# Kernel optimization log

Measured on AMD Instinct MI355X. Metric: run time of the kernel, lower is better.

Reference implementation:

```python
import jax, jax.numpy as jnp
import numpy as np

VOCAB, ENC, DEC, ATT, EMB = 10000, 2048, 512, 512, 512
B, P, L = 64, 196, 20


def setup_inputs() -> dict:
    key = jax.random.key(0)
    ks = jax.random.split(key, 24)
    s = lambda k, shape, fan: jax.random.normal(k, shape, jnp.float32) / np.sqrt(fan)
    inp = {
        "img_features": jax.random.normal(ks[0], (B, P, ENC), jnp.float32),
        "captions": jax.random.randint(ks[1], (B, L), 0, VOCAB),
        # init-state projections
        "W_init_h": s(ks[2], (DEC, ENC), ENC), "b_init_h": jnp.zeros((DEC,), jnp.float32),
        "W_init_c": s(ks[3], (DEC, ENC), ENC), "b_init_c": jnp.zeros((DEC,), jnp.float32),
        # attention
        "W_dec": s(ks[4], (ATT, DEC), DEC), "b_dec": jnp.zeros((ATT,), jnp.float32),
        "W_enc": s(ks[5], (ATT, ENC), ENC), "b_enc": jnp.zeros((ATT,), jnp.float32),
        "W_fin": s(ks[6], (1, ATT), ATT), "b_fin": jnp.zeros((1,), jnp.float32),
        # gate + output + embedding
        "W_gate": s(ks[7], (ENC, DEC), DEC), "b_gate": jnp.zeros((ENC,), jnp.float32),
        "W_out": s(ks[8], (VOCAB, DEC), DEC), "b_out": jnp.zeros((VOCAB,), jnp.float32),
        "emb": s(ks[9], (VOCAB, EMB), EMB),
        # LSTMCell (PyTorch gate order: i, f, g, o)
        "W_ih": s(ks[10], (4 * DEC, EMB + ENC), EMB + ENC), "b_ih": jnp.zeros((4 * DEC,), jnp.float32),
        "W_hh": s(ks[11], (4 * DEC, DEC), DEC), "b_hh": jnp.zeros((4 * DEC,), jnp.float32),
    }
    return inp


def _decode(img_features, captions, W_init_h, b_init_h, W_init_c, b_init_c,
            W_dec, b_dec, W_enc, b_enc, W_fin, b_fin,
            W_gate, b_gate, W_out, b_out, emb, W_ih, W_hh, b_ih, b_hh):
    # lengths are uniform (padded tensor), so sort/restore are identity and
    # batch_size_t == B at every step.
    avg = img_features.mean(axis=1)                              # [B,ENC]
    h0 = jnp.tanh(avg @ W_init_h.T + b_init_h)                   # [B,DEC]
    c0 = jnp.tanh(avg @ W_init_c.T + b_init_c)
    enc_proj = img_features @ W_enc.T + b_enc                    # [B,P,ATT] (loop-invariant)
    emb_seq = emb[captions[:, :-1]]                              # [B,T,EMB], T = L-1

    def step(carry, e_t):
        h, c = carry
        U_h = h @ W_dec.T + b_dec                                # [B,ATT]
        att = jnp.tanh(enc_proj + U_h[:, None, :])               # [B,P,ATT]
        e = (att @ W_fin.T + b_fin)[..., 0]                      # [B,P]
        alpha = jax.nn.softmax(e, axis=1)
        context = jnp.einsum('bpe,bp->be', img_features, alpha)  # [B,ENC]
        gate = jax.nn.sigmoid(h @ W_gate.T + b_gate)             # [B,ENC]
        x = jnp.concatenate([e_t, gate * context], axis=1)       # [B,EMB+ENC]
        gates = x @ W_ih.T + b_ih + h @ W_hh.T + b_hh            # [B,4*DEC]
        i, f, g, o = jnp.split(gates, 4, axis=1)
        c_new = jax.nn.sigmoid(f) * c + jax.nn.sigmoid(i) * jnp.tanh(g)
        h_new = jax.nn.sigmoid(o) * jnp.tanh(c_new)
        out = h_new @ W_out.T + b_out                            # [B,VOCAB] (dropout=eval identity)
        return (h_new, c_new), (out, alpha)

    _, (preds, alphas) = jax.lax.scan(step, (h0, c0), jnp.swapaxes(emb_seq, 0, 1))
    return jnp.swapaxes(preds, 0, 1), jnp.swapaxes(alphas, 0, 1)  # [B,T,VOCAB], [B,T,P]


def reference(img_features, captions, W_init_h, b_init_h, W_init_c, b_init_c,
              W_dec, b_dec, W_enc, b_enc, W_fin, b_fin,
              W_gate, b_gate, W_out, b_out, emb, W_ih, W_hh, b_ih, b_hh):
    return _decode(img_features, captions, W_init_h, b_init_h, W_init_c, b_init_c,
                   W_dec, b_dec, W_enc, b_enc, W_fin, b_fin,
                   W_gate, b_gate, W_out, b_out, emb, W_ih, W_hh, b_ih, b_hh)
```

## Files before the change

### kernel.cpp

```cpp
#include <hip/hip_runtime.h>
#include <hip/hip_bf16.h>

typedef unsigned short u16;
typedef unsigned int   u32;

#define BB    64
#define PP    196
#define ENC   2048
#define DEC   512
#define ATT   512
#define EMB   512
#define VOCAB 10000
#define VPAD2 10112
#define TT    19
#define LCAP  20
#define XDIM  3072
#define LDSTR 40
#define LD64  72

typedef __bf16 bf16x8 __attribute__((ext_vector_type(8)));
typedef float  f32x4  __attribute__((ext_vector_type(4)));

__device__ __forceinline__ float bf2f(u16 u) {
  union { float f; u32 i; } v; v.i = ((u32)u) << 16; return v.f;
}
__device__ __forceinline__ u16 f2bf(float f) {
  u32 x = __float_as_uint(f);
  u32 r = (x + 0x7FFFu + ((x >> 16) & 1u)) >> 16;
  return (u16)r;
}
__device__ __forceinline__ u32 pack2(float a, float b) {
  return (u32)f2bf(a) | ((u32)f2bf(b) << 16);
}
__device__ __forceinline__ float wred_sum(float v) {
  #pragma unroll
  for (int off = 32; off > 0; off >>= 1) v += __shfl_xor(v, off, 64);
  return v;
}
__device__ __forceinline__ float wred_max(float v) {
  #pragma unroll
  for (int off = 32; off > 0; off >>= 1) v = fmaxf(v, __shfl_xor(v, off, 64));
  return v;
}
__device__ __forceinline__ float tanh_fast(float x) {
  return 1.f - 2.f / (__expf(2.f * x) + 1.f);
}
__device__ __forceinline__ float sigm(float x) {
  return 1.f / (1.f + __expf(-x));
}

__global__ __launch_bounds__(256) void k_cvt_simple(u16* __restrict__ dst,
    const float* __restrict__ src, int n4) {
  int stride = gridDim.x * blockDim.x;
  for (int i = blockIdx.x * blockDim.x + threadIdx.x; i < n4; i += stride) {
    float4 v = ((const float4*)src)[i];
    ((uint2*)dst)[i] = make_uint2(pack2(v.x, v.y), pack2(v.z, v.w));
  }
}

__global__ __launch_bounds__(256) void k_cvt_pad(u16* __restrict__ dst,
    const float* __restrict__ src) {
  int total = VPAD2 * (DEC / 2);
  int stride = gridDim.x * blockDim.x;
  for (int i = blockIdx.x * blockDim.x + threadIdx.x; i < total; i += stride) {
    int row = i >> 8, c2 = i & 255;
    u32 v = 0;
    if (row < VOCAB) {
      float2 f = ((const float2*)src)[(size_t)row * 256 + c2];
      v = pack2(f.x, f.y);
    }
    ((u32*)dst)[i] = v;
  }
}

__global__ __launch_bounds__(256) void k_cvt_comb(u16* __restrict__ dst,
    const float* __restrict__ Wih, const float* __restrict__ Whh) {
  int j = blockIdx.x;
  for (int t = threadIdx.x; t < 768; t += 256) {
    int col = t * 4;
    float4 v = (col < 2560)
        ? ((const float4*)(Wih + (size_t)j * 2560))[t]
        : ((const float4*)(Whh + (size_t)j * 512))[(col - 2560) >> 2];
    ((uint2*)(dst + (size_t)j * XDIM))[t] = make_uint2(pack2(v.x, v.y), pack2(v.z, v.w));
  }
}

__global__ __launch_bounds__(256) void k_cvt_dect(u16* __restrict__ dst,
    const float* __restrict__ Wdec) {
  int idx = blockIdx.x * 256 + threadIdx.x;
  int k0 = idx >> 9, j = idx & 511;
  const float* src = Wdec + (size_t)j * DEC + k0 * 8;
  float4 f0 = ((const float4*)src)[0];
  float4 f1 = ((const float4*)src)[1];
  ((uint4*)dst)[idx] = make_uint4(pack2(f0.x, f0.y), pack2(f0.z, f0.w),
                                  pack2(f1.x, f1.y), pack2(f1.z, f1.w));
}

__global__ __launch_bounds__(256) void k_avg(const float* __restrict__ img,
    u16* __restrict__ avgb) {
  int b = blockIdx.x;
  int col = blockIdx.y * 256 + threadIdx.x;
  const float* base = img + (size_t)b * PP * ENC + col;
  float s = 0.f;
  for (int p = 0; p < PP; ++p) s += base[(size_t)p * ENC];
  avgb[b * ENC + col] = f2bf(s * (1.f / PP));
}

__global__ __launch_bounds__(256) void k_init_mfma(const u16* __restrict__ avgb,
    const u16* __restrict__ Winitb, const float* __restrict__ bh,
    const float* __restrict__ bc, u16* __restrict__ h, float* __restrict__ c) {
  __shared__ __align__(16) u16 As[2 * 64 * LD64];
  __shared__ __align__(16) u16 Bs[2 * 64 * LD64];
  int n0 = blockIdx.x * 64;
  int tid = threadIdx.x, wv = tid >> 6, lane = tid & 63;
  int wm = wv >> 1, wn = wv & 1;
  int fr = lane & 15, kg = (lane >> 4) * 8, rq = lane >> 4;
  int r0 = tid >> 3, kc0 = (tid & 7) * 8;
  int r1 = (tid + 256) >> 3, kc1 = ((tid + 256) & 7) * 8;
  uint4 pa0 = *(const uint4*)&avgb[(size_t)r0 * ENC + kc0];
  uint4 pa1 = *(const uint4*)&avgb[(size_t)r1 * ENC + kc1];
  uint4 pb0 = *(const uint4*)&Winitb[(size_t)(n0 + r0) * ENC + kc0];
  uint4 pb1 = *(const uint4*)&Winitb[(size_t)(n0 + r1) * ENC + kc1];
  f32x4 acc[2][2] = {};
  const int NK = ENC / 64;
  for (int kt = 0; kt < NK; ++kt) {
    u16* as = As + (kt & 1) * (64 * LD64);
    u16* bs = Bs + (kt & 1) * (64 * LD64);
    *(uint4*)&as[r0 * LD64 + kc0] = pa0;
    *(uint4*)&as[r1 * LD64 + kc1] = pa1;
    *(uint4*)&bs[r0 * LD64 + kc0] = pb0;
    *(uint4*)&bs[r1 * LD64 + kc1] = pb1;
    __syncthreads();
    if (kt + 1 < NK) {
      int k0 = (kt + 1) * 64;
      pa0 = *(const uint4*)&avgb[(size_t)r0 * ENC + k0 + kc0];
      pa1 = *(const uint4*)&avgb[(size_t)r1 * ENC + k0 + kc1];
      pb0 = *(const uint4*)&Winitb[(size_t)(n0 + r0) * ENC + k0 + kc0];
      pb1 = *(const uint4*)&Winitb[(size_t)(n0 + r1) * ENC + k0 + kc1];
    }
    #pragma unroll
    for (int ks = 0; ks < 2; ++ks) {
      bf16x8 a0 = *(const bf16x8*)&as[(wm * 32 + fr) * LD64 + ks * 32 + kg];
      bf16x8 a1 = *(const bf16x8*)&as[(wm * 32 + 16 + fr) * LD64 + ks * 32 + kg];
      bf16x8 b0 = *(const bf16x8*)&bs[(wn * 32 + fr) * LD64 + ks * 32 + kg];
      bf16x8 b1 = *(const bf16x8*)&bs[(wn * 32 + 16 + fr) * LD64 + ks * 32 + kg];
      acc[0][0] = __builtin_amdgcn_mfma_f32_16x16x32_bf16(a0, b0, acc[0][0], 0, 0, 0);
      acc[0][1] = __builtin_amdgcn_mfma_f32_16x16x32_bf16(a0, b1, acc[0][1], 0, 0, 0);
      acc[1][0] = __builtin_amdgcn_mfma_f32_16x16x32_bf16(a1, b0, acc[1][0], 0, 0, 0);
      acc[1][1] = __builtin_amdgcn_mfma_f32_16x16x32_bf16(a1, b1, acc[1][1], 0, 0, 0);
    }
  }
  #pragma unroll
  for (int mi = 0; mi < 2; ++mi)
    for (int ni = 0; ni < 2; ++ni)
      #pragma unroll
      for (int r = 0; r < 4; ++r) {
        int m = wm * 32 + mi * 16 + rq * 4 + r;
        int n = n0 + wn * 32 + ni * 16 + fr;
        float v = acc[mi][ni][r];
        if (n < DEC) h[m * DEC + n] = f2bf(tanh_fast(v + bh[n]));
        else         c[m * DEC + (n - DEC)] = tanh_fast(v + bc[n - DEC]);
      }
}

template <int SRC>
__global__ __launch_bounds__(256) void k_encproj(
    const u16* __restrict__ Ab, const float* __restrict__ Af,
    const u16* __restrict__ Wb, const float* __restrict__ Wf,
    const float* __restrict__ benc, u16* __restrict__ epj) {
  __shared__ __align__(16) u16 As[128 * LDSTR];
  __shared__ __align__(16) u16 Bs[128 * LDSTR];
  int m0 = blockIdx.x * 128, n0 = blockIdx.y * 128;
  int tid = threadIdx.x, wv = tid >> 6, lane = tid & 63;
  int wm = wv >> 1, wn = wv & 1;
  int fr = lane & 15, kg = (lane >> 4) * 8, rq = lane >> 4;
  f32x4 acc[4][4] = {};
  for (int k0 = 0; k0 < ENC; k0 += 32) {
    __syncthreads();
    #pragma unroll
    for (int i = 0; i < 2; ++i) {
      int id = tid + i * 256;
      int r = id >> 2, kc = id & 3;
      if (SRC == 0) {
        *(uint4*)(&As[r * LDSTR + kc * 8]) = *(const uint4*)(&Ab[(size_t)(m0 + r) * ENC + k0 + kc * 8]);
        *(uint4*)(&Bs[r * LDSTR + kc * 8]) = *(const uint4*)(&Wb[(size_t)(n0 + r) * ENC + k0 + kc * 8]);
      } else {
        const float* asrc = &Af[(size_t)(m0 + r) * ENC + k0 + kc * 8];
        float4 f0 = ((const float4*)asrc)[0];
        float4 f1 = ((const float4*)asrc)[1];
        *(uint4*)(&As[r * LDSTR + kc * 8]) =
            make_uint4(pack2(f0.x, f0.y), pack2(f0.z, f0.w),
                       pack2(f1.x, f1.y), pack2(f1.z, f1.w));
        const float* bsrc = &Wf[(size_t)(n0 + r) * ENC + k0 + kc * 8];
        float4 g0 = ((const float4*)bsrc)[0];
        float4 g1 = ((const float4*)bsrc)[1];
        *(uint4*)(&Bs[r * LDSTR + kc * 8]) =
            make_uint4(pack2(g0.x, g0.y), pack2(g0.z, g0.w),
                       pack2(g1.x, g1.y), pack2(g1.z, g1.w));
      }
    }
    __syncthreads();
    bf16x8 af[4], bfr[4];
    #pragma unroll
    for (int i = 0; i < 4; ++i) {
      af[i]  = *(const bf16x8*)(&As[(wm * 64 + i * 16 + fr) * LDSTR + kg]);
      bfr[i] = *(const bf16x8*)(&Bs[(wn * 64 + i * 16 + fr) * LDSTR + kg]);
    }
    #pragma unroll
    for (int mi = 0; mi < 4; ++mi)
      #pragma unroll
      for (int ni = 0; ni < 4; ++ni)
        acc[mi][ni] = __builtin_amdgcn_mfma_f32_16x16x32_bf16(af[mi], bfr[ni], acc[mi][ni], 0, 0, 0);
  }
  #pragma unroll
  for (int mi = 0; mi < 4; ++mi)
    for (int ni = 0; ni < 4; ++ni)
      #pragma unroll
      for (int r = 0; r < 4; ++r) {
        int m = m0 + wm * 64 + mi * 16 + rq * 4 + r;
        int n = n0 + wn * 64 + ni * 16 + fr;
        epj[(size_t)m * ATT + n] = f2bf(acc[mi][ni][r] + benc[n]);
      }
}

__global__ __launch_bounds__(256) void k_logits(const u16* __restrict__ hall,
    const u16* __restrict__ Woutb2, const float* __restrict__ bout,
    float* __restrict__ preds) {
  __shared__ __align__(16) u16 As[128 * LDSTR];
  __shared__ __align__(16) u16 Bs[128 * LDSTR];
  int m0 = blockIdx.x * 128, n0 = blockIdx.y * 128;
  int tid = threadIdx.x, wv = tid >> 6, lane = tid & 63;
  int wm = wv >> 1, wn = wv & 1;
  int fr = lane & 15, kg = (lane >> 4) * 8, rq = lane >> 4;
  f32x4 acc[4][4] = {};
  for (int k0 = 0; k0 < DEC; k0 += 32) {
    __syncthreads();
    #pragma unroll
    for (int i = 0; i < 2; ++i) {
      int id = tid + i * 256;
      int r = id >> 2, kc = id & 3;
      *(uint4*)(&As[r * LDSTR + kc * 8]) = *(const uint4*)(&hall[(size_t)(m0 + r) * DEC + k0 + kc * 8]);
      *(uint4*)(&Bs[r * LDSTR + kc * 8]) = *(const uint4*)(&Woutb2[(size_t)(n0 + r) * DEC + k0 + kc * 8]);
    }
    __syncthreads();
    bf16x8 af[4], bfr[4];
    #pragma unroll
    for (int i = 0; i < 4; ++i) {
      af[i]  = *(const bf16x8*)(&As[(wm * 64 + i * 16 + fr) * LDSTR + kg]);
      bfr[i] = *(const bf16x8*)(&Bs[(wn * 64 + i * 16 + fr) * LDSTR + kg]);
    }
    #pragma unroll
    for (int mi = 0; mi < 4; ++mi)
      #pragma unroll
      for (int ni = 0; ni < 4; ++ni)
        acc[mi][ni] = __builtin_amdgcn_mfma_f32_16x16x32_bf16(af[mi], bfr[ni], acc[mi][ni], 0, 0, 0);
  }
  #pragma unroll
  for (int mi = 0; mi < 4; ++mi)
    for (int ni = 0; ni < 4; ++ni)
      #pragma unroll
      for (int r = 0; r < 4; ++r) {
        int m = m0 + wm * 64 + mi * 16 + rq * 4 + r;
        int n = n0 + wn * 64 + ni * 16 + fr;
        if (m < TT * BB && n < VOCAB) {
          int t = m >> 6, b = m & 63;
          preds[(size_t)b * (TT * VOCAB) + (size_t)t * VOCAB + n] = acc[mi][ni][r] + bout[n];
        }
      }
}

__global__ __launch_bounds__(512) void k_front(const u16* __restrict__ h,
    const u16* __restrict__ WdecT2, const float* __restrict__ bdec,
    const u16* __restrict__ Wgateb, const float* __restrict__ bgate,
    const u16* __restrict__ epj, const float* __restrict__ wfin,
    const float* __restrict__ bfin, const int* __restrict__ captions,
    const float* __restrict__ emb,
    float* __restrict__ gate, float* __restrict__ e_ws,
    u16* __restrict__ x, float* __restrict__ alphas, int step) {
  __shared__ __align__(16) u16 smem[2 * 64 * LD64 + 2 * 128 * LD64];
  int bid = blockIdx.x;
  int tid = threadIdx.x, wv = tid >> 6, lane = tid & 63;

  if (bid >= 64) {
    u16* As = smem;
    u16* Bs = smem + 2 * 64 * LD64;
    int n0 = (bid - 64) * 128;
    int wm = wv >> 2, wn = wv & 3;
    int fr = lane & 15, kgr = (lane >> 4) * 8, rq = lane >> 4;
    int r0 = tid >> 3, kc0 = (tid & 7) * 8;
    uint4 pa  = *(const uint4*)&h[(size_t)r0 * DEC + kc0];
    uint4 pb0 = *(const uint4*)&Wgateb[(size_t)(n0 + r0) * DEC + kc0];
    uint4 pb1 = *(const uint4*)&Wgateb[(size_t)(n0 + 64 + r0) * DEC + kc0];
    f32x4 acc[2][2] = {};
    const int NK = DEC / 64;
    for (int kt = 0; kt < NK; ++kt) {
      u16* as = As + (kt & 1) * (64 * LD64);
      u16* bs = Bs + (kt & 1) * (128 * LD64);
      *(uint4*)&as[r0 * LD64 + kc0] = pa;
      *(uint4*)&bs[r0 * LD64 + kc0] = pb0;
      *(uint4*)&bs[(64 + r0) * LD64 + kc0] = pb1;
      __syncthreads();
      if (kt + 1 < NK) {
        int k0 = (kt + 1) * 64;
        pa  = *(const uint4*)&h[(size_t)r0 * DEC + k0 + kc0];
        pb0 = *(const uint4*)&Wgateb[(size_t)(n0 + r0) * DEC + k0 + kc0];
        pb1 = *(const uint4*)&Wgateb[(size_t)(n0 + 64 + r0) * DEC + k0 + kc0];
      }
      #pragma unroll
      for (int ks = 0; ks < 2; ++ks) {
        bf16x8 a0 = *(const bf16x8*)&as[(wm * 32 + fr) * LD64 + ks * 32 + kgr];
        bf16x8 a1 = *(const bf16x8*)&as[(wm * 32 + 16 + fr) * LD64 + ks * 32 + kgr];
        bf16x8 b0 = *(const bf16x8*)&bs[(wn * 32 + fr) * LD64 + ks * 32 + kgr];
        bf16x8 b1 = *(const bf16x8*)&bs[(wn * 32 + 16 + fr) * LD64 + ks * 32 + kgr];
        acc[0][0] = __builtin_amdgcn_mfma_f32_16x16x32_bf16(a0, b0, acc[0][0], 0, 0, 0);
        acc[0][1] = __builtin_amdgcn_mfma_f32_16x16x32_bf16(a0, b1, acc[0][1], 0, 0, 0);
        acc[1][0] = __builtin_amdgcn_mfma_f32_16x16x32_bf16(a1, b0, acc[1][0], 0, 0, 0);
        acc[1][1] = __builtin_amdgcn_mfma_f32_16x16x32_bf16(a1, b1, acc[1][1], 0, 0, 0);
      }
    }
    #pragma unroll
    for (int mi = 0; mi < 2; ++mi)
      for (int ni = 0; ni < 2; ++ni)
        #pragma unroll
        for (int r = 0; r < 4; ++r) {
          int m = wm * 32 + mi * 16 + rq * 4 + r;
          int n = n0 + wn * 32 + ni * 16 + fr;
          gate[m * ENC + n] = sigm(acc[mi][ni][r] + bgate[n]);
        }
    return;
  }

  float* s_h  = (float*)smem;
  float* s_uh = s_h + DEC;
  float* s_wf = s_uh + ATT;
  float* s_e  = s_wf + ATT;
  int b = bid;
  s_h[tid] = bf2f(h[b * DEC + tid]);
  s_wf[tid] = wfin[tid];
  if (tid < 256) {
    int capv = captions[b * LCAP + step];
    float2 f = ((const float2*)(emb + (size_t)capv * EMB))[tid];
    ((u32*)(x + (size_t)b * XDIM))[tid] = pack2(f.x, f.y);
    ((u32*)(x + (size_t)b * XDIM + 2560))[tid] = ((const u32*)(h + (size_t)b * DEC))[tid];
  }
  __syncthreads();
  {
    float acc = bdec[tid];
    #pragma unroll 4
    for (int k0 = 0; k0 < 64; ++k0) {
      bf16x8 wrow = *(const bf16x8*)&WdecT2[(size_t)(k0 * 512 + tid) * 8];
      #pragma unroll
      for (int kk = 0; kk < 8; ++kk)
        acc += s_h[k0 * 8 + kk] * (float)wrow[kk];
    }
    s_uh[tid] = acc;
  }
  __syncthreads();
  float b0 = bfin[0];
  for (int p = wv; p < PP; p += 8) {
    const u16* row = epj + (size_t)(b * PP + p) * ATT;
    float acc = 0.f;
    #pragma unroll
    for (int ki = 0; ki < 8; ++ki) {
      int a = lane + ki * 64;
      acc += tanh_fast(bf2f(row[a]) + s_uh[a]) * s_wf[a];
    }
    acc = wred_sum(acc);
    if (lane == 0) s_e[p] = acc + b0;
  }
  __syncthreads();
  if (tid < 64) {
    float v0 = s_e[tid], v1 = s_e[tid + 64], v2 = s_e[tid + 128];
    float v3 = (tid + 192 < PP) ? s_e[tid + 192] : -1e30f;
    float m = wred_max(fmaxf(fmaxf(v0, v1), fmaxf(v2, v3)));
    float e0 = __expf(v0 - m), e1 = __expf(v1 - m), e2 = __expf(v2 - m);
    float e3 = (tid + 192 < PP) ? __expf(v3 - m) : 0.f;
    float inv = 1.f / wred_sum(e0 + e1 + e2 + e3);
    s_e[tid] = e0 * inv; s_e[tid + 64] = e1 * inv; s_e[tid + 128] = e2 * inv;
    if (tid + 192 < PP) s_e[tid + 192] = e3 * inv;
  }
  __syncthreads();
  if (tid < PP) {
    float a = s_e[tid];
    alphas[(size_t)b * (TT * PP) + (size_t)step * PP + tid] = a;
    e_ws[b * PP + tid] = a;
  }
}

template <int SRC>
__global__ __launch_bounds__(256) void k_ctx(const float* __restrict__ e_ws,
    const float* __restrict__ gate, const u16* __restrict__ imgb,
    const float* __restrict__ imgf, u16* __restrict__ x) {
  __shared__ float s_a[PP];
  int b = blockIdx.x, et = blockIdx.y;
  int tid = threadIdx.x;
  if (tid < PP) s_a[tid] = e_ws[b * PP + tid];
  __syncthreads();
  int e0i = et * 512 + tid * 2;
  float c0 = 0.f, c1 = 0.f;
  if (SRC == 0) {
    const u16* ib = imgb + (size_t)b * PP * ENC + e0i;
    for (int p = 0; p < PP; ++p) {
      u32 v = *(const u32*)(ib + (size_t)p * ENC);
      float ap = s_a[p];
      c0 += ap * bf2f((u16)(v & 0xFFFF));
      c1 += ap * bf2f((u16)(v >> 16));
    }
  } else {
    const float* ib = imgf + (size_t)b * PP * ENC + e0i;
    for (int p = 0; p < PP; ++p) {
      float2 v = *(const float2*)(ib + (size_t)p * ENC);
      float ap = s_a[p];
      c0 += ap * v.x;
      c1 += ap * v.y;
    }
  }
  float g0 = gate[b * ENC + e0i], g1 = gate[b * ENC + e0i + 1];
  *(u32*)(&x[(size_t)b * XDIM + 512 + e0i]) = pack2(c0 * g0, c1 * g1);
}

__global__ __launch_bounds__(256) void k_lstm_part(const u16* __restrict__ x,
    const u16* __restrict__ Wcomb, float* __restrict__ pbuf) {
  __shared__ __align__(16) u16 As[2 * 64 * LD64];
  __shared__ __align__(16) u16 Bs[2 * 64 * LD64];
  int jt = blockIdx.x, ksp = blockIdx.y;
  int kbase = ksp * 768;
  int tid = threadIdx.x, wv = tid >> 6, lane = tid & 63;
  int wm = wv >> 1, wn = wv & 1;
  int fr = lane & 15, kg = (lane >> 4) * 8, rq = lane >> 4;
  int r0 = tid >> 3, kc0 = (tid & 7) * 8;
  int r1 = (tid + 256) >> 3, kc1 = ((tid + 256) & 7) * 8;
  int wrow0 = (r0 >> 4) * 512 + jt * 16 + (r0 & 15);
  int wrow1 = (r1 >> 4) * 512 + jt * 16 + (r1 & 15);
  uint4 pa0 = *(const uint4*)&x[(size_t)r0 * XDIM + kbase + kc0];
  uint4 pa1 = *(const uint4*)&x[(size_t)r1 * XDIM + kbase + kc1];
  uint4 pb0 = *(const uint4*)&Wcomb[(size_t)wrow0 * XDIM + kbase + kc0];
  uint4 pb1 = *(const uint4*)&Wcomb[(size_t)wrow1 * XDIM + kbase + kc1];
  f32x4 acc[2][2] = {};
  const int NK = 12;
  for (int kt = 0; kt < NK; ++kt) {
    u16* as = As + (kt & 1) * (64 * LD64);
    u16* bs = Bs + (kt & 1) * (64 * LD64);
    *(uint4*)&as[r0 * LD64 + kc0] = pa0;
    *(uint4*)&as[r1 * LD64 + kc1] = pa1;
    *(uint4*)&bs[r0 * LD64 + kc0] = pb0;
    *(uint4*)&bs[r1 * LD64 + kc1] = pb1;
    __syncthreads();
    if (kt + 1 < NK) {
      int k0 = kbase + (kt + 1) * 64;
      pa0 = *(const uint4*)&x[(size_t)r0 * XDIM + k0 + kc0];
      pa1 = *(const uint4*)&x[(size_t)r1 * XDIM + k0 + kc1];
      pb0 = *(const uint4*)&Wcomb[(size_t)wrow0 * XDIM + k0 + kc0];
      pb1 = *(const uint4*)&Wcomb[(size_t)wrow1 * XDIM + k0 + kc1];
    }
    #pragma unroll
    for (int ks = 0; ks < 2; ++ks) {
      bf16x8 a0 = *(const bf16x8*)&as[(wm * 32 + fr) * LD64 + ks * 32 + kg];
      bf16x8 a1 = *(const bf16x8*)&as[(wm * 32 + 16 + fr) * LD64 + ks * 32 + kg];
      bf16x8 b0 = *(const bf16x8*)&bs[(wn * 32 + fr) * LD64 + ks * 32 + kg];
      bf16x8 b1 = *(const bf16x8*)&bs[(wn * 32 + 16 + fr) * LD64 + ks * 32 + kg];
      acc[0][0] = __builtin_amdgcn_mfma_f32_16x16x32_bf16(a0, b0, acc[0][0], 0, 0, 0);
      acc[0][1] = __builtin_amdgcn_mfma_f32_16x16x32_bf16(a0, b1, acc[0][1], 0, 0, 0);
      acc[1][0] = __builtin_amdgcn_mfma_f32_16x16x32_bf16(a1, b0, acc[1][0], 0, 0, 0);
      acc[1][1] = __builtin_amdgcn_mfma_f32_16x16x32_bf16(a1, b1, acc[1][1], 0, 0, 0);
    }
  }
  float* pout = pbuf + (size_t)(ksp * 32 + jt) * 4096;
  #pragma unroll
  for (int mi = 0; mi < 2; ++mi)
    for (int ni = 0; ni < 2; ++ni)
      #pragma unroll
      for (int r = 0; r < 4; ++r) {
        int m = wm * 32 + mi * 16 + rq * 4 + r;
        int n = wn * 32 + ni * 16 + fr;
        pout[m * 64 + n] = acc[mi][ni][r];
      }
}

__global__ __launch_bounds__(256) void k_lstm_fin(const float* __restrict__ pbuf,
    const float* __restrict__ bih, const float* __restrict__ bhh,
    float* __restrict__ c, u16* __restrict__ h, u16* __restrict__ hall, int step) {
  int jt = blockIdx.x, tid = threadIdx.x;
  #pragma unroll
  for (int ii = 0; ii < 4; ++ii) {
    int idx = tid + ii * 256;
    int bb = idx >> 4, jj = idx & 15;
    int j = jt * 16 + jj;
    float g4[4];
    #pragma unroll
    for (int g = 0; g < 4; ++g) {
      float s = 0.f;
      #pragma unroll
      for (int ks = 0; ks < 4; ++ks)
        s += pbuf[(size_t)(ks * 32 + jt) * 4096 + bb * 64 + g * 16 + jj];
      g4[g] = s;
    }
    float iv = g4[0] + bih[j]        + bhh[j];
    float fv = g4[1] + bih[512 + j]  + bhh[512 + j];
    float gv = g4[2] + bih[1024 + j] + bhh[1024 + j];
    float ov = g4[3] + bih[1536 + j] + bhh[1536 + j];
    float co = c[bb * DEC + j];
    float cn = sigm(fv) * co + sigm(iv) * tanh_fast(gv);
    float hn = sigm(ov) * tanh_fast(cn);
    c[bb * DEC + j] = cn;
    u16 hb = f2bf(hn);
    h[bb * DEC + j] = hb;
    hall[(size_t)(step * BB + bb) * DEC + j] = hb;
  }
}

extern "C" void kernel_launch(void* const* d_in, const int* in_sizes, int n_in,
                              void* d_out, int out_size, void* d_ws, size_t ws_size,
                              hipStream_t stream) {
  const float* img   = (const float*)d_in[0];
  const int*   cap   = (const int*)  d_in[1];
  const float* Winh  = (const float*)d_in[2];
  const float* binh  = (const float*)d_in[3];
  const float* Winc  = (const float*)d_in[4];
  const float* binc  = (const float*)d_in[5];
  const float* Wdec  = (const float*)d_in[6];
  const float* bdec  = (const float*)d_in[7];
  const float* Wenc  = (const float*)d_in[8];
  const float* benc  = (const float*)d_in[9];
  const float* Wfin  = (const float*)d_in[10];
  const float* bfin  = (const float*)d_in[11];
  const float* Wgate = (const float*)d_in[12];
  const float* bgate = (const float*)d_in[13];
  const float* Wout  = (const float*)d_in[14];
  const float* bout  = (const float*)d_in[15];
  const float* emb   = (const float*)d_in[16];
  const float* Wih   = (const float*)d_in[17];
  const float* bih   = (const float*)d_in[18];
  const float* Whh   = (const float*)d_in[19];
  const float* bhh   = (const float*)d_in[20];

  char* ws = (char*)d_ws;
  u16*   epj    = (u16*)  (ws);
  u16*   Winitb = (u16*)  (ws);
  u16*   avgb   = (u16*)  (ws + 4194304);
  u16*   Wcomb  = (u16*)  (ws + 12845056);
  u16*   Woutb2 = (u16*)  (ws + 25427968);
  u16*   Wgateb = (u16*)  (ws + 35782656);
  u16*   WdecT2 = (u16*)  (ws + 37879808);
  u16*   Wencb  = (u16*)  (ws + 38404096);
  float* pbuf   = (float*)(ws + 40501248);
  u16*   h      = (u16*)  (ws + 42598400);
  float* c      = (float*)(ws + 42663936);
  float* e_ws   = (float*)(ws + 42795008);
  u16*   x      = (u16*)  (ws + 42846208);
  float* gate   = (float*)(ws + 43370496);
  u16*   hall   = (u16*)  (ws + 43894784);
  u16*   imgb   = (u16*)  (ws + 45205504);
  const bool use_imgb = (ws_size >= 96585728ull);

  float* preds  = (float*)d_out;
  float* alphas = (float*)d_out + (size_t)BB * TT * VOCAB;

  k_cvt_simple<<<512,  256, 0, stream>>>(Winitb,             Winh, 262144);
  k_cvt_simple<<<512,  256, 0, stream>>>(Winitb + 512 * ENC, Winc, 262144);
  if (use_imgb) {
    k_cvt_simple<<<4096, 256, 0, stream>>>(imgb,  img,  6422528);
    k_cvt_simple<<<512,  256, 0, stream>>>(Wencb, Wenc, 262144);
  }
  k_cvt_simple<<<512,  256, 0, stream>>>(Wgateb, Wgate, 262144);
  k_cvt_dect  <<<128,  256, 0, stream>>>(WdecT2, Wdec);
  k_cvt_pad   <<<2048, 256, 0, stream>>>(Woutb2, Wout);
  k_cvt_comb  <<<2048, 256, 0, stream>>>(Wcomb,  Wih, Whh);

  k_avg<<<dim3(BB, 8), 256, 0, stream>>>(img, avgb);
  k_init_mfma<<<16, 256, 0, stream>>>(avgb, Winitb, binh, binc, h, c);
  if (use_imgb)
    k_encproj<0><<<dim3(98, 4), 256, 0, stream>>>(imgb, img, Wencb, Wenc, benc, epj);
  else
    k_encproj<1><<<dim3(98, 4), 256, 0, stream>>>(imgb, img, Wencb, Wenc, benc, epj);

  for (int t = 0; t < TT; ++t) {
    k_front<<<80, 512, 0, stream>>>(h, WdecT2, bdec, Wgateb, bgate, epj, Wfin,
                                    bfin, cap, emb, gate, e_ws, x, alphas, t);
    if (use_imgb)
      k_ctx<0><<<dim3(BB, 4), 256, 0, stream>>>(e_ws, gate, imgb, img, x);
    else
      k_ctx<1><<<dim3(BB, 4), 256, 0, stream>>>(e_ws, gate, imgb, img, x);
    k_lstm_part<<<dim3(32, 4), 256, 0, stream>>>(x, Wcomb, pbuf);
    k_lstm_fin<<<32, 256, 0, stream>>>(pbuf, bih, bhh, c, h, hall, t);
  }
  k_logits<<<dim3(10, 79), 256, 0, stream>>>(hall, Woutb2, bout, preds);
}
```

Baseline: 1.234 ms.

## Fuse recurrent decode steps into one persistent kernel with grid barriers

Replaces the 76 per-step launches (front, ctx, lstm_part, lstm_fin for each of 19 steps) with one persistent 256-block kernel. It loops over timesteps and separates phases with a hierarchical atomic grid barrier. Blocks are reduced to 256 threads, so the front and gate phases get per-thread work doubling and retiling. This removes launch overhead and inter-kernel gaps on the serial recurrence. The cost is spin-wait barriers whose correctness depends on all 256 blocks being co-resident.

```diff
diff --git a/kernel.cpp b/kernel.cpp
--- a/kernel.cpp
+++ b/kernel.cpp
@@ -8,8 +8,8 @@
 #define PP    196
 #define ENC   2048
 #define DEC   512
+#define EMB   512
 #define ATT   512
-#define EMB   512
 #define VOCAB 10000
 #define VPAD2 10112
 #define TT    19
@@ -47,6 +47,29 @@
 }
 __device__ __forceinline__ float sigm(float x) {
   return 1.f / (1.f + __expf(-x));
+}
+
+__device__ __forceinline__ void grid_bar(u32* bar, u32 phase, int bid, int tid) {
+  __syncthreads();
+  if (tid == 0) {
+    __threadfence();
+    int g = bid >> 5;
+    u32 t = atomicAdd(&bar[g * 16], 1u) + 1u;
+    if (t == phase * 32u) {
+      u32 gt = atomicAdd(&bar[256], 1u) + 1u;
+      if (gt == phase * 8u) atomicAdd(&bar[272], 1u);
+      while (atomicAdd(&bar[272], 0u) < phase) __builtin_amdgcn_s_sleep(4);
+      atomicAdd(&bar[(8 + g) * 16], 1u);
+    } else {
+      while (atomicAdd(&bar[(8 + g) * 16], 0u) < phase) __builtin_amdgcn_s_sleep(4);
+    }
+    __threadfence();
+  }
+  __syncthreads();
+}
+
+__global__ void k_zero(u32* __restrict__ p) {
+  p[threadIdx.x + blockIdx.x * 256] = 0;
 }
 
 __global__ __launch_bounds__(256) void k_cvt_simple(u16* __restrict__ dst,
@@ -269,243 +292,261 @@
       }
 }
 
-__global__ __launch_bounds__(512) void k_front(const u16* __restrict__ h,
+template <int SRC>
+__global__ __launch_bounds__(256, 1) void k_loop(
+    u16* __restrict__ h, float* __restrict__ c,
     const u16* __restrict__ WdecT2, const float* __restrict__ bdec,
     const u16* __restrict__ Wgateb, const float* __restrict__ bgate,
     const u16* __restrict__ epj, const float* __restrict__ wfin,
     const float* __restrict__ bfin, const int* __restrict__ captions,
-    const float* __restrict__ emb,
-    float* __restrict__ gate, float* __restrict__ e_ws,
-    u16* __restrict__ x, float* __restrict__ alphas, int step) {
-  __shared__ __align__(16) u16 smem[2 * 64 * LD64 + 2 * 128 * LD64];
+    const float* __restrict__ emb, float* __restrict__ gate,
+    float* __restrict__ e_ws, u16* __restrict__ x,
+    const u16* __restrict__ imgb, const float* __restrict__ imgf,
+    const u16* __restrict__ Wcomb, float* __restrict__ pbuf,
+    const float* __restrict__ bih, const float* __restrict__ bhh,
+    u16* __restrict__ hall, float* __restrict__ alphas, u32* __restrict__ gbar) {
+  __shared__ __align__(16) u16 S[27648];
   int bid = blockIdx.x;
   int tid = threadIdx.x, wv = tid >> 6, lane = tid & 63;
-
-  if (bid >= 64) {
-    u16* As = smem;
-    u16* Bs = smem + 2 * 64 * LD64;
-    int n0 = (bid - 64) * 128;
-    int wm = wv >> 2, wn = wv & 3;
-    int fr = lane & 15, kgr = (lane >> 4) * 8, rq = lane >> 4;
-    int r0 = tid >> 3, kc0 = (tid & 7) * 8;
-    uint4 pa  = *(const uint4*)&h[(size_t)r0 * DEC + kc0];
-    uint4 pb0 = *(const uint4*)&Wgateb[(size_t)(n0 + r0) * DEC + kc0];
-    uint4 pb1 = *(const uint4*)&Wgateb[(size_t)(n0 + 64 + r0) * DEC + kc0];
-    f32x4 acc[2][2] = {};
-    const int NK = DEC / 64;
-    for (int kt = 0; kt < NK; ++kt) {
-      u16* as = As + (kt & 1) * (64 * LD64);
-      u16* bs = Bs + (kt & 1) * (128 * LD64);
-      *(uint4*)&as[r0 * LD64 + kc0] = pa;
-      *(uint4*)&bs[r0 * LD64 + kc0] = pb0;
-      *(uint4*)&bs[(64 + r0) * LD64 + kc0] = pb1;
+  u32 ph = 0;
+
+  for (int t = 0; t < TT; ++t) {
+    if (bid < 64) {
+      float* s_h  = (float*)S;
+      float* s_uh = s_h + DEC;
+      float* s_wf = s_uh + ATT;
+      float* s_e  = s_wf + ATT;
+      int b = bid;
+      s_h[tid] = bf2f(h[b * DEC + tid]);
+      s_h[tid + 256] = bf2f(h[b * DEC + tid + 256]);
+      s_wf[tid] = wfin[tid];
+      s_wf[tid + 256] = wfin[tid + 256];
+      {
+        int capv = captions[b * LCAP + t];
+        float2 f = ((const float2*)(emb + (size_t)capv * EMB))[tid];
+        ((u32*)(x + (size_t)b * XDIM))[tid] = pack2(f.x, f.y);
+        ((u32*)(x + (size_t)b * XDIM + 2560))[tid] = ((const u32*)(h + (size_t)b * DEC))[tid];
+      }
       __syncthreads();
-      if (kt + 1 < NK) {
-        int k0 = (kt + 1) * 64;
-        pa  = *(const uint4*)&h[(size_t)r0 * DEC + k0 + kc0];
-        pb0 = *(const uint4*)&Wgateb[(size_t)(n0 + r0) * DEC + k0 + kc0];
-        pb1 = *(const uint4*)&Wgateb[(size_t)(n0 + 64 + r0) * DEC + k0 + kc0];
-      }
-      #pragma unroll
-      for (int ks = 0; ks < 2; ++ks) {
-        bf16x8 a0 = *(const bf16x8*)&as[(wm * 32 + fr) * LD64 + ks * 32 + kgr];
-        bf16x8 a1 = *(const bf16x8*)&as[(wm * 32 + 16 + fr) * LD64 + ks * 32 + kgr];
-        bf16x8 b0 = *(const bf16x8*)&bs[(wn * 32 + fr) * LD64 + ks * 32 + kgr];
-        bf16x8 b1 = *(const bf16x8*)&bs[(wn * 32 + 16 + fr) * LD64 + ks * 32 + kgr];
-        acc[0][0] = __builtin_amdgcn_mfma_f32_16x16x32_bf16(a0, b0, acc[0][0], 0, 0, 0);
-        acc[0][1] = __builtin_amdgcn_mfma_f32_16x16x32_bf16(a0, b1, acc[0][1], 0, 0, 0);
-        acc[1][0] = __builtin_amdgcn_mfma_f32_16x16x32_bf16(a1, b0, acc[1][0], 0, 0, 0);
-        acc[1][1] = __builtin_amdgcn_mfma_f32_16x16x32_bf16(a1, b1, acc[1][1], 0, 0, 0);
-      }
-    }
-    #pragma unroll
-    for (int mi = 0; mi < 2; ++mi)
-      for (int ni = 0; ni < 2; ++ni)
+      {
+        float a0 = bdec[tid], a1 = bdec[tid + 256];
+        #pragma unroll 4
+        for (int k0 = 0; k0 < 64; ++k0) {
+          bf16x8 w0 = *(const bf16x8*)&WdecT2[(size_t)(k0 * 512 + tid) * 8];
+          bf16x8 w1 = *(const bf16x8*)&WdecT2[(size_t)(k0 * 512 + tid + 256) * 8];
+          #pragma unroll
+          for (int kk = 0; kk < 8; ++kk) {
+            float hv = s_h[k0 * 8 + kk];
+            a0 += hv * (float)w0[kk];
+            a1 += hv * (float)w1[kk];
+          }
+        }
+        s_uh[tid] = a0; s_uh[tid + 256] = a1;
+      }
+      __syncthreads();
+      float b0 = bfin[0];
+      for (int p = wv; p < PP; p += 4) {
+        const u16* row = epj + (size_t)(b * PP + p) * ATT;
+        float acc = 0.f;
         #pragma unroll
-        for (int r = 0; r < 4; ++r) {
-          int m = wm * 32 + mi * 16 + rq * 4 + r;
-          int n = n0 + wn * 32 + ni * 16 + fr;
-          gate[m * ENC + n] = sigm(acc[mi][ni][r] + bgate[n]);
-        }
-    return;
-  }
-
-  float* s_h  = (float*)smem;
-  float* s_uh = s_h + DEC;
-  float* s_wf = s_uh + ATT;
-  float* s_e  = s_wf + ATT;
-  int b = bid;
-  s_h[tid] = bf2f(h[b * DEC + tid]);
-  s_wf[tid] = wfin[tid];
-  if (tid < 256) {
-    int capv = captions[b * LCAP + step];
-    float2 f = ((const float2*)(emb + (size_t)capv * EMB))[tid];
-    ((u32*)(x + (size_t)b * XDIM))[tid] = pack2(f.x, f.y);
-    ((u32*)(x + (size_t)b * XDIM + 2560))[tid] = ((const u32*)(h + (size_t)b * DEC))[tid];
-  }
-  __syncthreads();
-  {
-    float acc = bdec[tid];
-    #pragma unroll 4
-    for (int k0 = 0; k0 < 64; ++k0) {
-      bf16x8 wrow = *(const bf16x8*)&WdecT2[(size_t)(k0 * 512 + tid) * 8];
-      #pragma unroll
-      for (int kk = 0; kk < 8; ++kk)
-        acc += s_h[k0 * 8 + kk] * (float)wrow[kk];
-    }
-    s_uh[tid] = acc;
-  }
-  __syncthreads();
-  float b0 = bfin[0];
-  for (int p = wv; p < PP; p += 8) {
-    const u16* row = epj + (size_t)(b * PP + p) * ATT;
-    float acc = 0.f;
-    #pragma unroll
-    for (int ki = 0; ki < 8; ++ki) {
-      int a = lane + ki * 64;
-      acc += tanh_fast(bf2f(row[a]) + s_uh[a]) * s_wf[a];
-    }
-    acc = wred_sum(acc);
-    if (lane == 0) s_e[p] = acc + b0;
-  }
-  __syncthreads();
-  if (tid < 64) {
-    float v0 = s_e[tid], v1 = s_e[tid + 64], v2 = s_e[tid + 128];
-    float v3 = (tid + 192 < PP) ? s_e[tid + 192] : -1e30f;
-    float m = wred_max(fmaxf(fmaxf(v0, v1), fmaxf(v2, v3)));
-    float e0 = __expf(v0 - m), e1 = __expf(v1 - m), e2 = __expf(v2 - m);
-    float e3 = (tid + 192 < PP) ? __expf(v3 - m) : 0.f;
-    float inv = 1.f / wred_sum(e0 + e1 + e2 + e3);
-    s_e[tid] = e0 * inv; s_e[tid + 64] = e1 * inv; s_e[tid + 128] = e2 * inv;
-    if (tid + 192 < PP) s_e[tid + 192] = e3 * inv;
-  }
-  __syncthreads();
-  if (tid < PP) {
-    float a = s_e[tid];
-    alphas[(size_t)b * (TT * PP) + (size_t)step * PP + tid] = a;
-    e_ws[b * PP + tid] = a;
-  }
-}
-
-template <int SRC>
-__global__ __launch_bounds__(256) void k_ctx(const float* __restrict__ e_ws,
-    const float* __restrict__ gate, const u16* __restrict__ imgb,
-    const float* __restrict__ imgf, u16* __restrict__ x) {
-  __shared__ float s_a[PP];
-  int b = blockIdx.x, et = blockIdx.y;
-  int tid = threadIdx.x;
-  if (tid < PP) s_a[tid] = e_ws[b * PP + tid];
-  __syncthreads();
-  int e0i = et * 512 + tid * 2;
-  float c0 = 0.f, c1 = 0.f;
-  if (SRC == 0) {
-    const u16* ib = imgb + (size_t)b * PP * ENC + e0i;
-    for (int p = 0; p < PP; ++p) {
-      u32 v = *(const u32*)(ib + (size_t)p * ENC);
-      float ap = s_a[p];
-      c0 += ap * bf2f((u16)(v & 0xFFFF));
-      c1 += ap * bf2f((u16)(v >> 16));
-    }
-  } else {
-    const float* ib = imgf + (size_t)b * PP * ENC + e0i;
-    for (int p = 0; p < PP; ++p) {
-      float2 v = *(const float2*)(ib + (size_t)p * ENC);
-      float ap = s_a[p];
-      c0 += ap * v.x;
-      c1 += ap * v.y;
-    }
-  }
-  float g0 = gate[b * ENC + e0i], g1 = gate[b * ENC + e0i + 1];
-  *(u32*)(&x[(size_t)b * XDIM + 512 + e0i]) = pack2(c0 * g0, c1 * g1);
-}
-
-__global__ __launch_bounds__(256) void k_lstm_part(const u16* __restrict__ x,
-    const u16* __restrict__ Wcomb, float* __restrict__ pbuf) {
-  __shared__ __align__(16) u16 As[2 * 64 * LD64];
-  __shared__ __align__(16) u16 Bs[2 * 64 * LD64];
-  int jt = blockIdx.x, ksp = blockIdx.y;
-  int kbase = ksp * 768;
-  int tid = threadIdx.x, wv = tid >> 6, lane = tid & 63;
-  int wm = wv >> 1, wn = wv & 1;
-  int fr = lane & 15, kg = (lane >> 4) * 8, rq = lane >> 4;
-  int r0 = tid >> 3, kc0 = (tid & 7) * 8;
-  int r1 = (tid + 256) >> 3, kc1 = ((tid + 256) & 7) * 8;
-  int wrow0 = (r0 >> 4) * 512 + jt * 16 + (r0 & 15);
-  int wrow1 = (r1 >> 4) * 512 + jt * 16 + (r1 & 15);
-  uint4 pa0 = *(const uint4*)&x[(size_t)r0 * XDIM + kbase + kc0];
-  uint4 pa1 = *(const uint4*)&x[(size_t)r1 * XDIM + kbase + kc1];
-  uint4 pb0 = *(const uint4*)&Wcomb[(size_t)wrow0 * XDIM + kbase + kc0];
-  uint4 pb1 = *(const uint4*)&Wcomb[(size_t)wrow1 * XDIM + kbase + kc1];
-  f32x4 acc[2][2] = {};
-  const int NK = 12;
-  for (int kt = 0; kt < NK; ++kt) {
-    u16* as = As + (kt & 1) * (64 * LD64);
-    u16* bs = Bs + (kt & 1) * (64 * LD64);
-    *(uint4*)&as[r0 * LD64 + kc0] = pa0;
-    *(uint4*)&as[r1 * LD64 + kc1] = pa1;
-    *(uint4*)&bs[r0 * LD64 + kc0] = pb0;
-    *(uint4*)&bs[r1 * LD64 + kc1] = pb1;
-    __syncthreads();
-    if (kt + 1 < NK) {
-      int k0 = kbase + (kt + 1) * 64;
-      pa0 = *(const uint4*)&x[(size_t)r0 * XDIM + k0 + kc0];
-      pa1 = *(const uint4*)&x[(size_t)r1 * XDIM + k0 + kc1];
-      pb0 = *(const uint4*)&Wcomb[(size_t)wrow0 * XDIM + k0 + kc0];
-      pb1 = *(const uint4*)&Wcomb[(size_t)wrow1 * XDIM + k0 + kc1];
-    }
-    #pragma unroll
-    for (int ks = 0; ks < 2; ++ks) {
-      bf16x8 a0 = *(const bf16x8*)&as[(wm * 32 + fr) * LD64 + ks * 32 + kg];
-      bf16x8 a1 = *(const bf16x8*)&as[(wm * 32 + 16 + fr) * LD64 + ks * 32 + kg];
-      bf16x8 b0 = *(const bf16x8*)&bs[(wn * 32 + fr) * LD64 + ks * 32 + kg];
-      bf16x8 b1 = *(const bf16x8*)&bs[(wn * 32 + 16 + fr) * LD64 + ks * 32 + kg];
-      acc[0][0] = __builtin_amdgcn_mfma_f32_16x16x32_bf16(a0, b0, acc[0][0], 0, 0, 0);
-      acc[0][1] = __builtin_amdgcn_mfma_f32_16x16x32_bf16(a0, b1, acc[0][1], 0, 0, 0);
-      acc[1][0] = __builtin_amdgcn_mfma_f32_16x16x32_bf16(a1, b0, acc[1][0], 0, 0, 0);
-      acc[1][1] = __builtin_amdgcn_mfma_f32_16x16x32_bf16(a1, b1, acc[1][1], 0, 0, 0);
-    }
-  }
-  float* pout = pbuf + (size_t)(ksp * 32 + jt) * 4096;
-  #pragma unroll
-  for (int mi = 0; mi < 2; ++mi)
-    for (int ni = 0; ni < 2; ++ni)
-      #pragma unroll
-      for (int r = 0; r < 4; ++r) {
-        int m = wm * 32 + mi * 16 + rq * 4 + r;
-        int n = wn * 32 + ni * 16 + fr;
-        pout[m * 64 + n] = acc[mi][ni][r];
-      }
-}
-
-__global__ __launch_bounds__(256) void k_lstm_fin(const float* __restrict__ pbuf,
-    const float* __restrict__ bih, const float* __restrict__ bhh,
-    float* __restrict__ c, u16* __restrict__ h, u16* __restrict__ hall, int step) {
-  int jt = blockIdx.x, tid = threadIdx.x;
-  #pragma unroll
-  for (int ii = 0; ii < 4; ++ii) {
-    int idx = tid + ii * 256;
-    int bb = idx >> 4, jj = idx & 15;
-    int j = jt * 16 + jj;
-    float g4[4];
-    #pragma unroll
-    for (int g = 0; g < 4; ++g) {
-      float s = 0.f;
-      #pragma unroll
-      for (int ks = 0; ks < 4; ++ks)
-        s += pbuf[(size_t)(ks * 32 + jt) * 4096 + bb * 64 + g * 16 + jj];
-      g4[g] = s;
-    }
-    float iv = g4[0] + bih[j]        + bhh[j];
-    float fv = g4[1] + bih[512 + j]  + bhh[512 + j];
-    float gv = g4[2] + bih[1024 + j] + bhh[1024 + j];
-    float ov = g4[3] + bih[1536 + j] + bhh[1536 + j];
-    float co = c[bb * DEC + j];
-    float cn = sigm(fv) * co + sigm(iv) * tanh_fast(gv);
-    float hn = sigm(ov) * tanh_fast(cn);
-    c[bb * DEC + j] = cn;
-    u16 hb = f2bf(hn);
-    h[bb * DEC + j] = hb;
-    hall[(size_t)(step * BB + bb) * DEC + j] = hb;
+        for (int ki = 0; ki < 8; ++ki) {
+          int a = lane + ki * 64;
+          acc += tanh_fast(bf2f(row[a]) + s_uh[a]) * s_wf[a];
+        }
+        acc = wred_sum(acc);
+        if (lane == 0) s_e[p] = acc + b0;
+      }
+      __syncthreads();
+      if (tid < 64) {
+        float v0 = s_e[tid], v1 = s_e[tid + 64], v2 = s_e[tid + 128];
+        float v3 = (tid + 192 < PP) ? s_e[tid + 192] : -1e30f;
+        float m = wred_max(fmaxf(fmaxf(v0, v1), fmaxf(v2, v3)));
+        float e0 = __expf(v0 - m), e1 = __expf(v1 - m), e2 = __expf(v2 - m);
+        float e3 = (tid + 192 < PP) ? __expf(v3 - m) : 0.f;
+        float inv = 1.f / wred_sum(e0 + e1 + e2 + e3);
+        s_e[tid] = e0 * inv; s_e[tid + 64] = e1 * inv; s_e[tid + 128] = e2 * inv;
+        if (tid + 192 < PP) s_e[tid + 192] = e3 * inv;
+      }
+      __syncthreads();
+      if (tid < PP) {
+        float a = s_e[tid];
+        alphas[(size_t)b * (TT * PP) + (size_t)t * PP + tid] = a;
+        e_ws[b * PP + tid] = a;
+      }
+    } else if (bid < 80) {
+      u16* As = S;
+      u16* Bs = S + 2 * 64 * LD64;
+      int n0 = (bid - 64) * 128;
+      int wm = wv >> 1, wn = wv & 1;
+      int fr = lane & 15, kgr = (lane >> 4) * 8, rq = lane >> 4;
+      int r0 = tid >> 3, kc0 = (tid & 7) * 8;
+      uint4 pa0 = *(const uint4*)&h[(size_t)r0 * DEC + kc0];
+      uint4 pa1 = *(const uint4*)&h[(size_t)(r0 + 32) * DEC + kc0];
+      uint4 pb0 = *(const uint4*)&Wgateb[(size_t)(n0 + r0) * DEC + kc0];
+      uint4 pb1 = *(const uint4*)&Wgateb[(size_t)(n0 + r0 + 32) * DEC + kc0];
+      uint4 pb2 = *(const uint4*)&Wgateb[(size_t)(n0 + r0 + 64) * DEC + kc0];
+      uint4 pb3 = *(const uint4*)&Wgateb[(size_t)(n0 + r0 + 96) * DEC + kc0];
+      f32x4 acc[2][4] = {};
+      const int NK = DEC / 64;
+      for (int kt = 0; kt < NK; ++kt) {
+        u16* as = As + (kt & 1) * (64 * LD64);
+        u16* bs = Bs + (kt & 1) * (128 * LD64);
+        *(uint4*)&as[r0 * LD64 + kc0] = pa0;
+        *(uint4*)&as[(r0 + 32) * LD64 + kc0] = pa1;
+        *(uint4*)&bs[r0 * LD64 + kc0] = pb0;
+        *(uint4*)&bs[(r0 + 32) * LD64 + kc0] = pb1;
+        *(uint4*)&bs[(r0 + 64) * LD64 + kc0] = pb2;
+        *(uint4*)&bs[(r0 + 96) * LD64 + kc0] = pb3;
+        __syncthreads();
+        if (kt + 1 < NK) {
+          int k0 = (kt + 1) * 64;
+          pa0 = *(const uint4*)&h[(size_t)r0 * DEC + k0 + kc0];
+          pa1 = *(const uint4*)&h[(size_t)(r0 + 32) * DEC + k0 + kc0];
+          pb0 = *(const uint4*)&Wgateb[(size_t)(n0 + r0) * DEC + k0 + kc0];
+          pb1 = *(const uint4*)&Wgateb[(size_t)(n0 + r0 + 32) * DEC + k0 + kc0];
+          pb2 = *(const uint4*)&Wgateb[(size_t)(n0 + r0 + 64) * DEC + k0 + kc0];
+          pb3 = *(const uint4*)&Wgateb[(size_t)(n0 + r0 + 96) * DEC + k0 + kc0];
+        }
+        #pragma unroll
+        for (int ks = 0; ks < 2; ++ks) {
+          bf16x8 a0 = *(const bf16x8*)&as[(wm * 32 + fr) * LD64 + ks * 32 + kgr];
+          bf16x8 a1 = *(const bf16x8*)&as[(wm * 32 + 16 + fr) * LD64 + ks * 32 + kgr];
+          #pragma unroll
+          for (int ni = 0; ni < 4; ++ni) {
+            bf16x8 bv = *(const bf16x8*)&bs[(wn * 64 + ni * 16 + fr) * LD64 + ks * 32 + kgr];
+            acc[0][ni] = __builtin_amdgcn_mfma_f32_16x16x32_bf16(a0, bv, acc[0][ni], 0, 0, 0);
+            acc[1][ni] = __builtin_amdgcn_mfma_f32_16x16x32_bf16(a1, bv, acc[1][ni], 0, 0, 0);
+          }
+        }
+      }
+      #pragma unroll
+      for (int mi = 0; mi < 2; ++mi)
+        for (int ni = 0; ni < 4; ++ni)
+          #pragma unroll
+          for (int r = 0; r < 4; ++r) {
+            int m = wm * 32 + mi * 16 + rq * 4 + r;
+            int n = n0 + wn * 64 + ni * 16 + fr;
+            gate[m * ENC + n] = sigm(acc[mi][ni][r] + bgate[n]);
+          }
+    }
+    ph++; grid_bar(gbar, ph, bid, tid);
+
+    {
+      float* s_a = (float*)S;
+      int b = bid >> 2, et = bid & 3;
+      if (tid < PP) s_a[tid] = e_ws[b * PP + tid];
+      __syncthreads();
+      int e0i = et * 512 + tid * 2;
+      float c0 = 0.f, c1 = 0.f;
+      if (SRC == 0) {
+        const u16* ib = imgb + (size_t)b * PP * ENC + e0i;
+        for (int p = 0; p < PP; ++p) {
+          u32 v = *(const u32*)(ib + (size_t)p * ENC);
+          float ap = s_a[p];
+          c0 += ap * bf2f((u16)(v & 0xFFFF));
+          c1 += ap * bf2f((u16)(v >> 16));
+        }
+      } else {
+        const float* ib = imgf + (size_t)b * PP * ENC + e0i;
+        for (int p = 0; p < PP; ++p) {
+          float2 v = *(const float2*)(ib + (size_t)p * ENC);
+          float ap = s_a[p];
+          c0 += ap * v.x;
+          c1 += ap * v.y;
+        }
+      }
+      float g0 = gate[b * ENC + e0i], g1 = gate[b * ENC + e0i + 1];
+      *(u32*)(&x[(size_t)b * XDIM + 512 + e0i]) = pack2(c0 * g0, c1 * g1);
+      __syncthreads();
+    }
+    ph++; grid_bar(gbar, ph, bid, tid);
+
+    if (bid < 128) {
+      u16* As = S;
+      u16* Bs = S + 2 * 64 * LD64;
+      int jt = bid & 31, ksp = bid >> 5;
+      int kbase = ksp * 768;
+      int wm = wv >> 1, wn = wv & 1;
+      int fr = lane & 15, kgr = (lane >> 4) * 8, rq = lane >> 4;
+      int r0 = tid >> 2, kc0 = (tid & 3) * 8;
+      int kc1 = kc0 + 32;
+      int wrow0 = (r0 >> 4) * 512 + jt * 16 + (r0 & 15);
+      uint4 pa0 = *(const uint4*)&x[(size_t)r0 * XDIM + kbase + kc0];
+      uint4 pa1 = *(const uint4*)&x[(size_t)r0 * XDIM + kbase + kc1];
+      uint4 pb0 = *(const uint4*)&Wcomb[(size_t)wrow0 * XDIM + kbase + kc0];
+      uint4 pb1 = *(const uint4*)&Wcomb[(size_t)wrow0 * XDIM + kbase + kc1];
+      f32x4 acc[2][2] = {};
+      const int NK = 12;
+      for (int kt = 0; kt < NK; ++kt) {
+        u16* as = As + (kt & 1) * (64 * LD64);
+        u16* bs = Bs + (kt & 1) * (64 * LD64);
+        *(uint4*)&as[r0 * LD64 + kc0] = pa0;
+        *(uint4*)&as[r0 * LD64 + kc1] = pa1;
+        *(uint4*)&bs[r0 * LD64 + kc0] = pb0;
+        *(uint4*)&bs[r0 * LD64 + kc1] = pb1;
+        __syncthreads();
+        if (kt + 1 < NK) {
+          int k0 = kbase + (kt + 1) * 64;
+          pa0 = *(const uint4*)&x[(size_t)r0 * XDIM + k0 + kc0];
+          pa1 = *(const uint4*)&x[(size_t)r0 * XDIM + k0 + kc1];
+          pb0 = *(const uint4*)&Wcomb[(size_t)wrow0 * XDIM + k0 + kc0];
+          pb1 = *(const uint4*)&Wcomb[(size_t)wrow0 * XDIM + k0 + kc1];
+        }
+        #pragma unroll
+        for (int ks = 0; ks < 2; ++ks) {
+          bf16x8 a0 = *(const bf16x8*)&as[(wm * 32 + fr) * LD64 + ks * 32 + kgr];
+          bf16x8 a1 = *(const bf16x8*)&as[(wm * 32 + 16 + fr) * LD64 + ks * 32 + kgr];
+          bf16x8 b0 = *(const bf16x8*)&bs[(wn * 32 + fr) * LD64 + ks * 32 + kgr];
+          bf16x8 b1 = *(const bf16x8*)&bs[(wn * 32 + 16 + fr) * LD64 + ks * 32 + kgr];
+          acc[0][0] = __builtin_amdgcn_mfma_f32_16x16x32_bf16(a0, b0, acc[0][0], 0, 0, 0);
+          acc[0][1] = __builtin_amdgcn_mfma_f32_16x16x32_bf16(a0, b1, acc[0][1], 0, 0, 0);
+          acc[1][0] = __builtin_amdgcn_mfma_f32_16x16x32_bf16(a1, b0, acc[1][0], 0, 0, 0);
+          acc[1][1] = __builtin_amdgcn_mfma_f32_16x16x32_bf16(a1, b1, acc[1][1], 0, 0, 0);
+        }
+      }
+      float* pout = pbuf + (size_t)(ksp * 32 + jt) * 4096;
+      #pragma unroll
+      for (int mi = 0; mi < 2; ++mi)
+        for (int ni = 0; ni < 2; ++ni)
+          #pragma unroll
+          for (int r = 0; r < 4; ++r) {
+            int m = wm * 32 + mi * 16 + rq * 4 + r;
+            int n = wn * 32 + ni * 16 + fr;
+            pout[m * 64 + n] = acc[mi][ni][r];
+          }
+    }
+    ph++; grid_bar(gbar, ph, bid, tid);
+
+    if (bid < 32) {
+      int jt = bid;
+      #pragma unroll
+      for (int ii = 0; ii < 4; ++ii) {
+        int idx = tid + ii * 256;
+        int bb = idx >> 4, jj = idx & 15;
+        int j = jt * 16 + jj;
+        float g4[4];
+        #pragma unroll
+        for (int g = 0; g < 4; ++g) {
+          float s = 0.f;
+          #pragma unroll
+          for (int ks = 0; ks < 4; ++ks)
+            s += pbuf[(size_t)(ks * 32 + jt) * 4096 + bb * 64 + g * 16 + jj];
+          g4[g] = s;
+        }
+        float iv = g4[0] + bih[j]        + bhh[j];
+        float fv = g4[1] + bih[512 + j]  + bhh[512 + j];
+        float gv = g4[2] + bih[1024 + j] + bhh[1024 + j];
+        float ov = g4[3] + bih[1536 + j] + bhh[1536 + j];
+        float co = c[bb * DEC + j];
+        float cn = sigm(fv) * co + sigm(iv) * tanh_fast(gv);
+        float hn = sigm(ov) * tanh_fast(cn);
+        c[bb * DEC + j] = cn;
+        u16 hb = f2bf(hn);
+        h[bb * DEC + j] = hb;
+        hall[(size_t)(t * BB + bb) * DEC + j] = hb;
+      }
+    }
+    ph++; grid_bar(gbar, ph, bid, tid);
   }
 }
 
@@ -548,6 +589,7 @@
   float* c      = (float*)(ws + 42663936);
   float* e_ws   = (float*)(ws + 42795008);
   u16*   x      = (u16*)  (ws + 42846208);
+  u32*   gbar   = (u32*)  (ws + 43239424);
   float* gate   = (float*)(ws + 43370496);
   u16*   hall   = (u16*)  (ws + 43894784);
   u16*   imgb   = (u16*)  (ws + 45205504);
@@ -556,6 +598,7 @@
   float* preds  = (float*)d_out;
   float* alphas = (float*)d_out + (size_t)BB * TT * VOCAB;
 
+  k_zero<<<4, 256, 0, stream>>>(gbar);
   k_cvt_simple<<<512,  256, 0, stream>>>(Winitb,             Winh, 262144);
   k_cvt_simple<<<512,  256, 0, stream>>>(Winitb + 512 * ENC, Winc, 262144);
   if (use_imgb) {
@@ -574,15 +617,14 @@
   else
     k_encproj<1><<<dim3(98, 4), 256, 0, stream>>>(imgb, img, Wencb, Wenc, benc, epj);
 
-  for (int t = 0; t < TT; ++t) {
-    k_front<<<80, 512, 0, stream>>>(h, WdecT2, bdec, Wgateb, bgate, epj, Wfin,
-                                    bfin, cap, emb, gate, e_ws, x, alphas, t);
-    if (use_imgb)
-      k_ctx<0><<<dim3(BB, 4), 256, 0, stream>>>(e_ws, gate, imgb, img, x);
-    else
-      k_ctx<1><<<dim3(BB, 4), 256, 0, stream>>>(e_ws, gate, imgb, img, x);
-    k_lstm_part<<<dim3(32, 4), 256, 0, stream>>>(x, Wcomb, pbuf);
-    k_lstm_fin<<<32, 256, 0, stream>>>(pbuf, bih, bhh, c, h, hall, t);
-  }
+  if (use_imgb)
+    k_loop<0><<<256, 256, 0, stream>>>(h, c, WdecT2, bdec, Wgateb, bgate, epj,
+        Wfin, bfin, cap, emb, gate, e_ws, x, imgb, img, Wcomb, pbuf, bih, bhh,
+        hall, alphas, gbar);
+  else
+    k_loop<1><<<256, 256, 0, stream>>>(h, c, WdecT2, bdec, Wgateb, bgate, epj,
+        Wfin, bfin, cap, emb, gate, e_ws, x, imgb, img, Wcomb, pbuf, bih, bhh,
+        hall, alphas, gbar);
+
   k_logits<<<dim3(10, 79), 256, 0, stream>>>(hall, Woutb2, bout, preds);
 }
```

Result: slower. 4.356 ms (+252.8%).
